# Optimization experiments

Measured on AMD Instinct MI355X. Metric: run time of the kernel, lower is better.

Reference implementation:

```python
import jax, jax.numpy as jnp
import numpy as np

EP, T1, N, H, OUT = 512, 1024, 128, 256, 64  # epcho, t_1(=bs), input_size, hidden_size, output_size


def setup_inputs() -> dict:
    key = jax.random.key(0)
    ks = jax.random.split(key, 9)
    w = lambda k, shape: jax.random.normal(k, shape, dtype=jnp.float32) * 0.05
    return dict(
        input=jax.random.normal(ks[0], (EP, T1, N), dtype=jnp.float32),
        hidden=jnp.zeros((1, T1, H), dtype=jnp.float32),  # (n_layers, bs, hidden)
        W_ih=w(ks[1], (3 * H, N)),   # GRU weight_ih_l0 (r,z,n gates stacked)
        W_hh=w(ks[2], (3 * H, H)),   # GRU weight_hh_l0
        b_ih=w(ks[3], (3 * H,)),
        b_hh=w(ks[4], (3 * H,)),
        W_hr=w(ks[5], (N, H)),
        b_hr=w(ks[6], (N,)),
        W_reg=w(ks[7], (OUT, T1)),
        b_reg=w(ks[8], (OUT,)),
    )


def reference(input, hidden, W_ih, W_hh, b_ih, b_hh, W_hr, b_hr, W_reg, b_reg):
    # Sequential GRU recurrence over the epcho axis; each step is a GRUCell with
    # batch = t_1 and seq_len = 1 (exactly what the torch loop computes).
    h0 = hidden[0]  # (T1, H) -- single layer

    def step(h, x):  # h: (T1, H), x: (T1, N)
        gi = x @ W_ih.T + b_ih            # (T1, 3H)
        gh = h @ W_hh.T + b_hh            # (T1, 3H)
        i_r, i_z, i_n = jnp.split(gi, 3, axis=-1)
        h_r, h_z, h_n = jnp.split(gh, 3, axis=-1)
        r = jax.nn.sigmoid(i_r + h_r)
        z = jax.nn.sigmoid(i_z + h_z)
        n_t = jnp.tanh(i_n + r * h_n)
        h_new = (1.0 - z) * n_t + z * h   # (T1, H)
        out = (h_new @ W_hr.T + b_hr).T
        return h_new, out

    _, outputs = jax.lax.scan(step, h0, input)  # (EP, N, T1)
    return outputs @ W_reg.T + b_reg            # (EP, N, OUT)
```

## Files before the change

### kernel.cpp

```cpp
#include <hip/hip_runtime.h>
#include <hip/hip_bf16.h>

#define EPN  512
#define T1N  1024
#define NIN  128
#define HSN  256
#define OUTN 64
#define NBLK 256
#define NTHR 256

typedef __attribute__((ext_vector_type(8))) short bf16x8;
typedef __attribute__((ext_vector_type(4))) short bf16x4;
typedef __attribute__((ext_vector_type(4))) float f32x4;
typedef __attribute__((ext_vector_type(4))) unsigned int u32x4;

struct KArgs {
  const float *x, *h0, *W_ih, *W_hh, *b_ih, *b_hh, *W_hr, *b_hr, *W_reg, *b_reg;
  float *out;
  ushort *hb;
  float *Ppart;
  float *Pbuf;
  float *Sreg;
  unsigned int *hflags;
  unsigned int *pflags;
};

__device__ __forceinline__ float sigm(float v) { return 1.f / (1.f + __expf(-v)); }
__device__ __forceinline__ float tanh_fast(float v) { return 2.f / (1.f + __expf(-2.f * v)) - 1.f; }
__device__ __forceinline__ short f2bf(float f) {
  return (short)__builtin_bit_cast(ushort, __float2bfloat16(f));
}
__device__ __forceinline__ bf16x8 cvt8(f32x4 a, f32x4 b) {
  bf16x8 r;
  r[0]=f2bf(a[0]); r[1]=f2bf(a[1]); r[2]=f2bf(a[2]); r[3]=f2bf(a[3]);
  r[4]=f2bf(b[0]); r[5]=f2bf(b[1]); r[6]=f2bf(b[2]); r[7]=f2bf(b[3]);
  return r;
}

__device__ __forceinline__ bf16x8 ld16h_sc(const ushort* p) {
  bf16x8 v; asm volatile("global_load_dwordx4 %0, %1, off sc0 sc1" : "=v"(v) : "v"(p)); return v;
}
__device__ __forceinline__ f32x4 ld16f_sc(const float* p) {
  f32x4 v; asm volatile("global_load_dwordx4 %0, %1, off sc0 sc1" : "=v"(v) : "v"(p)); return v;
}
__device__ __forceinline__ u32x4 ld16u_sc(const unsigned int* p) {
  u32x4 v; asm volatile("global_load_dwordx4 %0, %1, off sc0 sc1" : "=v"(v) : "v"(p)); return v;
}
__device__ __forceinline__ float ld4f_sc(const float* p) {
  float v; asm volatile("global_load_dword %0, %1, off sc0 sc1" : "=v"(v) : "v"(p)); return v;
}
__device__ __forceinline__ void st16f_sc(float* p, f32x4 v) {
  asm volatile("global_store_dwordx4 %0, %1, off sc0 sc1" :: "v"(p), "v"(v) : "memory");
}
__device__ __forceinline__ void st8h_sc(ushort* p, bf16x4 v) {
  asm volatile("global_store_dwordx2 %0, %1, off sc0 sc1" :: "v"(p), "v"(v) : "memory");
}
__device__ __forceinline__ void st4f_sc(float* p, float v) {
  asm volatile("global_store_dword %0, %1, off sc0 sc1" :: "v"(p), "v"(v) : "memory");
}
__device__ __forceinline__ void st4u_sc(unsigned int* p, unsigned int v) {
  asm volatile("global_store_dword %0, %1, off sc0 sc1" :: "v"(p), "v"(v) : "memory");
}
__device__ __forceinline__ f32x4 ld16f(const float* p) {
  f32x4 v; asm volatile("global_load_dwordx4 %0, %1, off" : "=v"(v) : "v"(p)); return v;
}
#define WAITV0 do { asm volatile("s_waitcnt vmcnt(0)" ::: "memory"); \
                    __builtin_amdgcn_sched_barrier(0); } while (0)

__device__ __forceinline__ unsigned int min4(u32x4 v) {
  unsigned int m = v[0];
  m = v[1] < m ? v[1] : m; m = v[2] < m ? v[2] : m; m = v[3] < m ? v[3] : m;
  return m;
}
__device__ __forceinline__ void waitflags(const unsigned int* f, int nquad,
                                          unsigned int target, int tid) {
  if (tid < 64) {
    int spins = 0;
    for (;;) {
      unsigned int m = 0xFFFFFFFFu;
      if (tid < nquad) m = min4(ld16u_sc(f + tid * 4));
      asm volatile("s_waitcnt vmcnt(0)" ::: "memory");
      if (__all((int)(m >= target))) break;
      if (++spins > (1 << 17)) break;
      __builtin_amdgcn_s_sleep(2);
    }
  }
  __syncthreads();
}

#define MFMA(A,B,C) __builtin_amdgcn_mfma_f32_16x16x32_bf16(A, B, C, 0, 0, 0)

__global__ void gru_setup(KArgs a) {
  const int gtid = blockIdx.x * blockDim.x + threadIdx.x;
  const int gsz = gridDim.x * blockDim.x;
  if (gtid < 512) { if (gtid < 256) a.hflags[gtid] = 0; else a.pflags[gtid - 256] = 0; }
  for (int i = gtid; i < T1N * HSN; i += gsz)
    a.hb[i] = __builtin_bit_cast(ushort, __float2bfloat16(a.h0[i]));
  if (gtid < OUTN) {
    float ssum = 0.f; const float* wr = a.W_reg + (size_t)gtid * T1N;
    for (int t = 0; t < T1N; ++t) ssum += wr[t];
    a.Sreg[gtid] = ssum;
  }
}

__global__ __launch_bounds__(NTHR, 1) void gru6(KArgs a) {
  const int bid = blockIdx.x, tid = threadIdx.x;

  const int tgrp = bid & 15, cgrp = bid >> 4;
  const int t0 = tgrp * 64, c0 = cgrp * 16;

  __shared__ __align__(16) short WtL[64 * 80];
  __shared__ __align__(16) short hT [16 * 80];
  __shared__ float cpart[256];

  {
    int o = tid >> 2, seg = tid & 3;
    const float* wr = a.W_reg + (size_t)o * T1N + t0 + seg * 16;
    bf16x8 p0, p1;
    #pragma unroll
    for (int j = 0; j < 8; ++j) p0[j] = f2bf(wr[j]);
    #pragma unroll
    for (int j = 0; j < 8; ++j) p1[j] = f2bf(wr[8 + j]);
    *(bf16x8*)&WtL[o * 80 + seg * 16]     = p0;
    *(bf16x8*)&WtL[o * 80 + seg * 16 + 8] = p1;
  }
  __syncthreads();

  const int lane = tid & 63, wv_ = tid >> 6;
  const int cl = lane & 15, kg = lane >> 4;
  const int tb = t0 + wv_ * 16;
  const int c  = c0 + cl;
  const float bR  = a.b_ih[c] + a.b_hh[c];
  const float bZ  = a.b_ih[HSN + c] + a.b_hh[HSN + c];
  const float bIN = a.b_ih[2*HSN + c];
  const float bHN = a.b_hh[2*HSN + c];

  bf16x8 whR[8], whZ[8], whN[8];
  #pragma unroll
  for (int ks = 0; ks < 8; ++ks) {
    const float* pr = a.W_hh + (size_t)(0*HSN + c) * HSN + ks * 32 + kg * 8;
    const float* pz = a.W_hh + (size_t)(1*HSN + c) * HSN + ks * 32 + kg * 8;
    const float* pn = a.W_hh + (size_t)(2*HSN + c) * HSN + ks * 32 + kg * 8;
    whR[ks] = cvt8(*(const f32x4*)pr, *(const f32x4*)(pr + 4));
    whZ[ks] = cvt8(*(const f32x4*)pz, *(const f32x4*)(pz + 4));
    whN[ks] = cvt8(*(const f32x4*)pn, *(const f32x4*)(pn + 4));
  }
  bf16x8 wxR[4], wxZ[4], wxN[4];
  #pragma unroll
  for (int ks = 0; ks < 4; ++ks) {
    const float* pr = a.W_ih + (size_t)(0*HSN + c) * NIN + ks * 32 + kg * 8;
    const float* pz = a.W_ih + (size_t)(1*HSN + c) * NIN + ks * 32 + kg * 8;
    const float* pn = a.W_ih + (size_t)(2*HSN + c) * NIN + ks * 32 + kg * 8;
    wxR[ks] = cvt8(*(const f32x4*)pr, *(const f32x4*)(pr + 4));
    wxZ[ks] = cvt8(*(const f32x4*)pz, *(const f32x4*)(pz + 4));
    wxN[ks] = cvt8(*(const f32x4*)pn, *(const f32x4*)(pn + 4));
  }

  const int n0 = bid >> 1, oh = (bid & 1) * 32;
  const int oo = tid & 31, part = tid >> 5;
  f32x4 whr[8];
  #pragma unroll
  for (int j = 0; j < 8; ++j) whr[j] = *(const f32x4*)&a.W_hr[(size_t)n0 * HSN + part * 32 + j * 4];
  const float cb = a.b_hr[n0];
  const float sregv = a.Sreg[oh + oo];
  const float bregv = a.b_reg[oh + oo];

  float hp[4];
  #pragma unroll
  for (int r = 0; r < 4; ++r) hp[r] = a.h0[(size_t)(tb + kg * 4 + r) * HSN + c];

  f32x4 giR = {0,0,0,0}, giZ = {0,0,0,0}, giN = {0,0,0,0};
  {
    const float* xrow = a.x + (size_t)(tb + cl) * NIN + kg * 8;
    #pragma unroll
    for (int ks = 0; ks < 4; ++ks) {
      f32x4 x0 = *(const f32x4*)(xrow + ks * 32);
      f32x4 x1 = *(const f32x4*)(xrow + ks * 32 + 4);
      bf16x8 af = cvt8(x0, x1);
      giR = MFMA(af, wxR[ks], giR); giZ = MFMA(af, wxZ[ks], giZ); giN = MFMA(af, wxN[ks], giN);
    }
  }

  for (int s = 0; s < EPN + 2; ++s) {
    const ushort* hb_r = a.hb + (size_t)(s & 1) * (T1N * HSN);
    ushort*       hb_w = a.hb + (size_t)((s + 1) & 1) * (T1N * HSN);

    if (s >= 1 && s < EPN) waitflags(a.hflags + tgrp * 16, 4, (unsigned)s, tid);

    bf16x8 hfr[8];
    if (s < EPN) {
      const ushort* hrow = hb_r + (size_t)(tb + cl) * HSN + kg * 8;
      #pragma unroll
      for (int ks = 0; ks < 8; ++ks) hfr[ks] = ld16h_sc(hrow + ks * 32);
    }
    f32x4 xa[4], xb[4];
    const bool hasX = (s + 1 < EPN);
    if (hasX) {
      const float* xrow = a.x + ((size_t)(s + 1) * T1N + tb + cl) * NIN + kg * 8;
      #pragma unroll
      for (int ks = 0; ks < 4; ++ks) {
        xa[ks] = ld16f(xrow + ks * 32);
        xb[ks] = ld16f(xrow + ks * 32 + 4);
      }
    }
    WAITV0;

    if (s < EPN) {
      f32x4 accR = {0,0,0,0}, accZ = {0,0,0,0}, accN = {0,0,0,0};
      #pragma unroll
      for (int ks = 0; ks < 8; ++ks) {
        accR = MFMA(hfr[ks], whR[ks], accR);
        accZ = MFMA(hfr[ks], whZ[ks], accZ);
        accN = MFMA(hfr[ks], whN[ks], accN);
      }
      bf16x4 hpk;
      #pragma unroll
      for (int r = 0; r < 4; ++r) {
        float rr = sigm(accR[r] + giR[r] + bR);
        float zz = sigm(accZ[r] + giZ[r] + bZ);
        float nn = tanh_fast(giN[r] + bIN + rr * (accN[r] + bHN));
        float hn = (1.f - zz) * nn + zz * hp[r];
        hp[r] = hn;
        hpk[r] = f2bf(hn);
      }
      *(bf16x4*)&hT[cl * 80 + wv_ * 16 + kg * 4] = hpk;
    }
    __syncthreads();

    if (s < EPN) {
      int th = tid >> 2, c4 = (tid & 3) * 4;
      bf16x4 hpk2;
      #pragma unroll
      for (int j = 0; j < 4; ++j) hpk2[j] = hT[(c4 + j) * 80 + th];
      st8h_sc(hb_w + (size_t)(t0 + th) * HSN + c0 + c4, hpk2);
    }
    WAITV0;
    __syncthreads();
    if (s < EPN && tid == 0) st4u_sc(a.hflags + tgrp * 16 + cgrp, (unsigned)(s + 1));

    f32x4 giR2 = {0,0,0,0}, giZ2 = {0,0,0,0}, giN2 = {0,0,0,0};
    if (hasX) {
      #pragma unroll
      for (int ks = 0; ks < 4; ++ks) {
        bf16x8 af = cvt8(xa[ks], xb[ks]);
        giR2 = MFMA(af, wxR[ks], giR2); giZ2 = MFMA(af, wxZ[ks], giZ2); giN2 = MFMA(af, wxN[ks], giN2);
      }
    }
    giR = giR2; giZ = giZ2; giN = giN2;

    if (s >= 1) waitflags(a.pflags, 64, (unsigned)s, tid);

    float rv[16];
    if (tid < 64 && s >= 1 && s <= EPN) {
      const float* pp = a.Ppart + (size_t)((s - 1) & 1) * (16 * 16384) + bid * 64 + tid;
      #pragma unroll
      for (int j = 0; j < 16; ++j) rv[j] = ld4f_sc(pp + (size_t)j * 16384);
    }
    f32x4 cv[8];
    if (s >= 2) {
      const float* pb = a.Pbuf + (size_t)((s - 1) & 1) * 16384 + (size_t)(oh + oo) * 256 + part * 32;
      #pragma unroll
      for (int j = 0; j < 8; ++j) cv[j] = ld16f_sc(pb + j * 4);
    }
    WAITV0;
    if (s < EPN) {
      f32x4 pacc = {0,0,0,0};
      #pragma unroll
      for (int ks = 0; ks < 2; ++ks) {
        bf16x8 pa = *(const bf16x8*)&hT[cl * 80 + ks * 32 + kg * 8];
        bf16x8 pb = *(const bf16x8*)&WtL[(wv_ * 16 + cl) * 80 + ks * 32 + kg * 8];
        pacc = MFMA(pa, pb, pacc);
      }
      st16f_sc(a.Ppart + ((size_t)(s & 1) * 16 + tgrp) * 16384 + (size_t)(wv_ * 16 + cl) * 256 + c0 + kg * 4, pacc);
    }
    if (tid < 64 && s >= 1 && s <= EPN) {
      float sum = 0.f;
      #pragma unroll
      for (int j = 0; j < 16; ++j) sum += rv[j];
      st4f_sc(a.Pbuf + (size_t)(s & 1) * 16384 + bid * 64 + tid, sum);
    }
    if (s >= 2) {
      float cacc = 0.f;
      #pragma unroll
      for (int j = 0; j < 8; ++j)
        cacc += whr[j][0]*cv[j][0] + whr[j][1]*cv[j][1] + whr[j][2]*cv[j][2] + whr[j][3]*cv[j][3];
      cpart[part * 32 + oo] = cacc;
    }
    __syncthreads();
    if (s >= 2 && tid < 32) {
      float v = cb * sregv + bregv;
      #pragma unroll
      for (int p = 0; p < 8; ++p) v += cpart[p * 32 + tid];
      st4f_sc(a.out + ((size_t)(s - 2) * NIN + n0) * OUTN + oh + tid, v);
    }

    WAITV0;
    __syncthreads();
    if (tid == 0) st4u_sc(a.pflags + bid, (unsigned)(s + 1));
  }
}

extern "C" void kernel_launch(void* const* d_in, const int* in_sizes, int n_in,
                              void* d_out, int out_size, void* d_ws, size_t ws_size,
                              hipStream_t stream) {
  KArgs a;
  a.x     = (const float*)d_in[0];
  a.h0    = (const float*)d_in[1];
  a.W_ih  = (const float*)d_in[2];
  a.W_hh  = (const float*)d_in[3];
  a.b_ih  = (const float*)d_in[4];
  a.b_hh  = (const float*)d_in[5];
  a.W_hr  = (const float*)d_in[6];
  a.b_hr  = (const float*)d_in[7];
  a.W_reg = (const float*)d_in[8];
  a.b_reg = (const float*)d_in[9];
  a.out   = (float*)d_out;

  char* w = (char*)d_ws;
  a.hb     = (ushort*)w;       w += (size_t)2 * T1N * HSN * 2;
  a.Ppart  = (float*)w;        w += (size_t)2 * 16 * 16384 * 4;
  a.Pbuf   = (float*)w;        w += (size_t)2 * 16384 * 4;
  a.Sreg   = (float*)w;        w += 256;
  a.hflags = (unsigned int*)w; w += 256 * 4;
  a.pflags = (unsigned int*)w; w += 256 * 4;

  hipLaunchKernelGGL(gru_setup, dim3(64), dim3(NTHR), 0, stream, a);
  hipLaunchKernelGGL(gru6, dim3(NBLK), dim3(NTHR), 0, stream, a);
}
```

Measured before the change: 3.830 ms.

## Deepen output-projection pipeline to four stages with bf16 partials and release flags

Extends the cross-block reduction pipeline for the hidden-regressor partials from two to four buffered stages. Each step now waits on the partial flags from two steps earlier instead of the current step, which takes the global barrier off the recurrence critical path. Partials are stored as bf16 to halve reduction traffic, flags are published with system-scope release atomic stores, and the spin sleep on the h-flag wait is shortened. The costs are more workspace, lower precision in the partial sums, and two extra loop iterations at the end.

Result: slower. 6.122 ms (+59.8%).

```diff
diff --git a/kernel.cpp b/kernel.cpp
--- a/kernel.cpp
+++ b/kernel.cpp
@@ -18,7 +18,7 @@
   const float *x, *h0, *W_ih, *W_hh, *b_ih, *b_hh, *W_hr, *b_hr, *W_reg, *b_reg;
   float *out;
   ushort *hb;
-  float *Ppart;
+  ushort *Ppart;
   float *Pbuf;
   float *Sreg;
   unsigned int *hflags;
@@ -46,11 +46,8 @@
 __device__ __forceinline__ u32x4 ld16u_sc(const unsigned int* p) {
   u32x4 v; asm volatile("global_load_dwordx4 %0, %1, off sc0 sc1" : "=v"(v) : "v"(p)); return v;
 }
-__device__ __forceinline__ float ld4f_sc(const float* p) {
-  float v; asm volatile("global_load_dword %0, %1, off sc0 sc1" : "=v"(v) : "v"(p)); return v;
-}
-__device__ __forceinline__ void st16f_sc(float* p, f32x4 v) {
-  asm volatile("global_store_dwordx4 %0, %1, off sc0 sc1" :: "v"(p), "v"(v) : "memory");
+__device__ __forceinline__ unsigned int ld2h_sc(const ushort* p) {
+  unsigned int v; asm volatile("global_load_ushort %0, %1, off sc0 sc1" : "=v"(v) : "v"(p)); return v;
 }
 __device__ __forceinline__ void st8h_sc(ushort* p, bf16x4 v) {
   asm volatile("global_store_dwordx2 %0, %1, off sc0 sc1" :: "v"(p), "v"(v) : "memory");
@@ -58,20 +55,22 @@
 __device__ __forceinline__ void st4f_sc(float* p, float v) {
   asm volatile("global_store_dword %0, %1, off sc0 sc1" :: "v"(p), "v"(v) : "memory");
 }
-__device__ __forceinline__ void st4u_sc(unsigned int* p, unsigned int v) {
-  asm volatile("global_store_dword %0, %1, off sc0 sc1" :: "v"(p), "v"(v) : "memory");
-}
 __device__ __forceinline__ f32x4 ld16f(const float* p) {
   f32x4 v; asm volatile("global_load_dwordx4 %0, %1, off" : "=v"(v) : "v"(p)); return v;
 }
 #define WAITV0 do { asm volatile("s_waitcnt vmcnt(0)" ::: "memory"); \
                     __builtin_amdgcn_sched_barrier(0); } while (0)
+
+__device__ __forceinline__ void publish(unsigned int* p, unsigned int v) {
+  __hip_atomic_store(p, v, __ATOMIC_RELEASE, __HIP_MEMORY_SCOPE_SYSTEM);
+}
 
 __device__ __forceinline__ unsigned int min4(u32x4 v) {
   unsigned int m = v[0];
   m = v[1] < m ? v[1] : m; m = v[2] < m ? v[2] : m; m = v[3] < m ? v[3] : m;
   return m;
 }
+template<int SLP>
 __device__ __forceinline__ void waitflags(const unsigned int* f, int nquad,
                                           unsigned int target, int tid) {
   if (tid < 64) {
@@ -82,7 +81,7 @@
       asm volatile("s_waitcnt vmcnt(0)" ::: "memory");
       if (__all((int)(m >= target))) break;
       if (++spins > (1 << 17)) break;
-      __builtin_amdgcn_s_sleep(2);
+      __builtin_amdgcn_s_sleep(SLP);
     }
   }
   __syncthreads();
@@ -103,7 +102,7 @@
   }
 }
 
-__global__ __launch_bounds__(NTHR, 1) void gru6(KArgs a) {
+__global__ __launch_bounds__(NTHR, 1) void gru9(KArgs a) {
   const int bid = blockIdx.x, tid = threadIdx.x;
 
   const int tgrp = bid & 15, cgrp = bid >> 4;
@@ -181,11 +180,11 @@
     }
   }
 
-  for (int s = 0; s < EPN + 2; ++s) {
+  for (int s = 0; s < EPN + 4; ++s) {
     const ushort* hb_r = a.hb + (size_t)(s & 1) * (T1N * HSN);
     ushort*       hb_w = a.hb + (size_t)((s + 1) & 1) * (T1N * HSN);
 
-    if (s >= 1 && s < EPN) waitflags(a.hflags + tgrp * 16, 4, (unsigned)s, tid);
+    if (s >= 1 && s < EPN) waitflags<1>(a.hflags + tgrp * 16, 4, (unsigned)s, tid);
 
     bf16x8 hfr[8];
     if (s < EPN) {
@@ -236,7 +235,23 @@
     }
     WAITV0;
     __syncthreads();
-    if (s < EPN && tid == 0) st4u_sc(a.hflags + tgrp * 16 + cgrp, (unsigned)(s + 1));
+    if (s < EPN && tid == 0) publish(a.hflags + tgrp * 16 + cgrp, (unsigned)(s + 1));
+
+    if (s >= 2) waitflags<2>(a.pflags, 64, (unsigned)(s - 1), tid);
+
+    unsigned int rv[16];
+    const bool hasR = (s >= 2 && s < EPN + 2);
+    if (tid < 64 && hasR) {
+      const ushort* pp = a.Ppart + (size_t)((s - 2) & 3) * (16 * 16384) + bid * 64 + tid;
+      #pragma unroll
+      for (int j = 0; j < 16; ++j) rv[j] = ld2h_sc(pp + (size_t)j * 16384);
+    }
+    f32x4 cv[8];
+    if (s >= 4) {
+      const float* pb = a.Pbuf + (size_t)((s - 4) & 3) * 16384 + (size_t)(oh + oo) * 256 + part * 32;
+      #pragma unroll
+      for (int j = 0; j < 8; ++j) cv[j] = ld16f_sc(pb + j * 4);
+    }
 
     f32x4 giR2 = {0,0,0,0}, giZ2 = {0,0,0,0}, giN2 = {0,0,0,0};
     if (hasX) {
@@ -247,22 +262,8 @@
       }
     }
     giR = giR2; giZ = giZ2; giN = giN2;
-
-    if (s >= 1) waitflags(a.pflags, 64, (unsigned)s, tid);
-
-    float rv[16];
-    if (tid < 64 && s >= 1 && s <= EPN) {
-      const float* pp = a.Ppart + (size_t)((s - 1) & 1) * (16 * 16384) + bid * 64 + tid;
-      #pragma unroll
-      for (int j = 0; j < 16; ++j) rv[j] = ld4f_sc(pp + (size_t)j * 16384);
-    }
-    f32x4 cv[8];
-    if (s >= 2) {
-      const float* pb = a.Pbuf + (size_t)((s - 1) & 1) * 16384 + (size_t)(oh + oo) * 256 + part * 32;
-      #pragma unroll
-      for (int j = 0; j < 8; ++j) cv[j] = ld16f_sc(pb + j * 4);
-    }
     WAITV0;
+
     if (s < EPN) {
       f32x4 pacc = {0,0,0,0};
       #pragma unroll
@@ -271,15 +272,18 @@
         bf16x8 pb = *(const bf16x8*)&WtL[(wv_ * 16 + cl) * 80 + ks * 32 + kg * 8];
         pacc = MFMA(pa, pb, pacc);
       }
-      st16f_sc(a.Ppart + ((size_t)(s & 1) * 16 + tgrp) * 16384 + (size_t)(wv_ * 16 + cl) * 256 + c0 + kg * 4, pacc);
-    }
-    if (tid < 64 && s >= 1 && s <= EPN) {
+      bf16x4 pk;
+      #pragma unroll
+      for (int r = 0; r < 4; ++r) pk[r] = f2bf(pacc[r]);
+      st8h_sc(a.Ppart + ((size_t)(s & 3) * 16 + tgrp) * 16384 + (size_t)(wv_ * 16 + cl) * 256 + c0 + kg * 4, pk);
+    }
+    if (tid < 64 && hasR) {
       float sum = 0.f;
       #pragma unroll
-      for (int j = 0; j < 16; ++j) sum += rv[j];
-      st4f_sc(a.Pbuf + (size_t)(s & 1) * 16384 + bid * 64 + tid, sum);
-    }
-    if (s >= 2) {
+      for (int j = 0; j < 16; ++j) sum += __builtin_bit_cast(float, rv[j] << 16);
+      st4f_sc(a.Pbuf + (size_t)((s - 2) & 3) * 16384 + bid * 64 + tid, sum);
+    }
+    if (s >= 4) {
       float cacc = 0.f;
       #pragma unroll
       for (int j = 0; j < 8; ++j)
@@ -287,16 +291,16 @@
       cpart[part * 32 + oo] = cacc;
     }
     __syncthreads();
-    if (s >= 2 && tid < 32) {
+    if (s >= 4 && tid < 32) {
       float v = cb * sregv + bregv;
       #pragma unroll
       for (int p = 0; p < 8; ++p) v += cpart[p * 32 + tid];
-      st4f_sc(a.out + ((size_t)(s - 2) * NIN + n0) * OUTN + oh + tid, v);
+      st4f_sc(a.out + ((size_t)(s - 4) * NIN + n0) * OUTN + oh + tid, v);
     }
 
     WAITV0;
     __syncthreads();
-    if (tid == 0) st4u_sc(a.pflags + bid, (unsigned)(s + 1));
+    if (tid == 0) publish(a.pflags + bid, (unsigned)(s + 1));
   }
 }
 
@@ -317,13 +321,13 @@
   a.out   = (float*)d_out;
 
   char* w = (char*)d_ws;
-  a.hb     = (ushort*)w;       w += (size_t)2 * T1N * HSN * 2;
-  a.Ppart  = (float*)w;        w += (size_t)2 * 16 * 16384 * 4;
-  a.Pbuf   = (float*)w;        w += (size_t)2 * 16384 * 4;
-  a.Sreg   = (float*)w;        w += 256;
   a.hflags = (unsigned int*)w; w += 256 * 4;
   a.pflags = (unsigned int*)w; w += 256 * 4;
+  a.Sreg   = (float*)w;        w += 256;
+  a.hb     = (ushort*)w;       w += (size_t)2 * T1N * HSN * 2;
+  a.Pbuf   = (float*)w;        w += (size_t)4 * 16384 * 4;
+  a.Ppart  = (ushort*)w;       w += (size_t)4 * 16 * 16384 * 2;
 
   hipLaunchKernelGGL(gru_setup, dim3(64), dim3(NTHR), 0, stream, a);
-  hipLaunchKernelGGL(gru6, dim3(NBLK), dim3(NTHR), 0, stream, a);
-}
+  hipLaunchKernelGGL(gru9, dim3(NBLK), dim3(NTHR), 0, stream, a);
+}
```
